# Kernel optimization log

Measured on AMD Instinct MI355X. Metric: run time of the kernel, lower is better.

The kernel has to match this reference:

```python
import jax, jax.numpy as jnp
import numpy as np

B, Q, F, D, H = 16384, 1024, 2, 5, 4  # batch, n_qubits, n_features, depth, heads


def setup_inputs() -> dict:
    key = jax.random.key(0)
    ks = iter(jax.random.split(key, 16))
    def rnd(shape, s=0.02):
        return jax.random.normal(next(ks), shape, dtype=jnp.float32) * s
    return {
        "x": jax.random.normal(next(ks), (B, F), dtype=jnp.float32),
        # amplitude_encoder: Linear(F,4Q) -> LN -> GELU -> Linear(4Q,2Q) -> LN -> Tanh -> Linear(2Q,Q)
        "amp_W1": rnd((4 * Q, F)), "amp_b1": jnp.zeros((4 * Q,), jnp.float32),
        "amp_g1": jnp.ones((4 * Q,), jnp.float32), "amp_be1": jnp.zeros((4 * Q,), jnp.float32),
        "amp_W2": rnd((2 * Q, 4 * Q)), "amp_b2": jnp.zeros((2 * Q,), jnp.float32),
        "amp_g2": jnp.ones((2 * Q,), jnp.float32), "amp_be2": jnp.zeros((2 * Q,), jnp.float32),
        "amp_W3": rnd((Q, 2 * Q)), "amp_b3": jnp.zeros((Q,), jnp.float32),
        # phase_encoder: Linear(F,2Q) -> LN -> SiLU -> Linear(2Q,Q) -> Tanh
        "ph_W1": rnd((2 * Q, F)), "ph_b1": jnp.zeros((2 * Q,), jnp.float32),
        "ph_g1": jnp.ones((2 * Q,), jnp.float32), "ph_be1": jnp.zeros((2 * Q,), jnp.float32),
        "ph_W2": rnd((Q, 2 * Q)), "ph_b2": jnp.zeros((Q,), jnp.float32),
        # rotation parameters (depth, Q, 3); only the last depth slice survives the overwrite loop
        "rot_freq": jax.random.normal(next(ks), (D, Q, 3), dtype=jnp.float32),
        "rot_phase": jax.random.normal(next(ks), (D, Q, 3), dtype=jnp.float32),
        # MultiheadAttention(Q, 4 heads)
        "attn_in_w": rnd((3 * Q, Q)), "attn_in_b": jnp.zeros((3 * Q,), jnp.float32),
        "attn_out_w": rnd((Q, Q)), "attn_out_b": jnp.zeros((Q,), jnp.float32),
    }


def _ln(x, g, b):
    m = jnp.mean(x, -1, keepdims=True)
    v = jnp.mean((x - m) ** 2, -1, keepdims=True)
    return (x - m) * jax.lax.rsqrt(v + 1e-5) * g + b


def reference(x, amp_W1, amp_b1, amp_g1, amp_be1, amp_W2, amp_b2, amp_g2, amp_be2,
              amp_W3, amp_b3, ph_W1, ph_b1, ph_g1, ph_be1, ph_W2, ph_b2,
              rot_freq, rot_phase, attn_in_w, attn_in_b, attn_out_w, attn_out_b):
    # amplitude encoder (Dropout is identity in eval mode)
    h = jax.nn.gelu(_ln(x @ amp_W1.T + amp_b1, amp_g1, amp_be1), approximate=False)
    h = jnp.tanh(_ln(h @ amp_W2.T + amp_b2, amp_g2, amp_be2))
    amp = h @ amp_W3.T + amp_b3                      # (B, Q)
    # phase encoder
    p = jax.nn.silu(_ln(x @ ph_W1.T + ph_b1, ph_g1, ph_be1))
    phase = jnp.tanh(p @ ph_W2.T + ph_b2)            # (B, Q)
    # multiscale conv branch: n_features=2 < min kernel size 3 => skipped, combined_conv = 0
    # depth loop overwrites quantum_state each iteration => only depth index D-1 matters
    rx = jnp.sin(amp * rot_freq[-1, :, 0] + rot_phase[-1, :, 0])
    ry = jnp.cos(phase * rot_freq[-1, :, 1] + rot_phase[-1, :, 1])
    rz = jnp.broadcast_to(jnp.tanh(rot_phase[-1, :, 2]), rx.shape)  # tanh(0*f + p)
    qs = (rx + ry + rz) / 3.0                        # (B, Q)
    # MultiheadAttention with seq_len == 1: softmax over a single key is exactly 1,
    # so attended output == V projection regardless of Q/K.
    qkv = qs @ attn_in_w.T + attn_in_b               # (B, 3Q)
    v = qkv[:, 2 * Q:]                               # (B, Q)
    return v @ attn_out_w.T + attn_out_b
```

## Files before the change

### kernel.cpp

```cpp
#include <hip/hip_runtime.h>

using bf16x8 = __attribute__((ext_vector_type(8))) __bf16;
using u16x8  = __attribute__((ext_vector_type(8))) unsigned short;
using f32x4  = __attribute__((ext_vector_type(4))) float;

__device__ __forceinline__ unsigned short f2bf(float f){
  unsigned int u = __float_as_uint(f);
  u += 0x7fffu + ((u >> 16) & 1u);
  return (unsigned short)(u >> 16);
}
__device__ __forceinline__ float bf2f(unsigned short h){
  return __uint_as_float(((unsigned int)h) << 16);
}

__global__ __launch_bounds__(256) void cvt_bf16(const float* __restrict__ s,
                                                unsigned short* __restrict__ d, int n){
  int i = blockIdx.x * 256 + threadIdx.x;
  if (i < n) d[i] = f2bf(s[i]);
}

__global__ __launch_bounds__(256) void front_amp_kernel(
    const float* __restrict__ x,
    const float* __restrict__ W1, const float* __restrict__ b1,
    const float* __restrict__ g1, const float* __restrict__ be1,
    unsigned short* __restrict__ h)
{
  __shared__ float red[256];
  __shared__ float red2[256];
  __shared__ float s_mean, s_inv;
  const int row = blockIdx.x;
  const int tid = threadIdx.x;
  const float x0 = x[row * 2 + 0];
  const float x1 = x[row * 2 + 1];

  const f32x4* W4 = (const f32x4*)(W1 + (size_t)tid * 32);
  float va[16];
  float sum = 0.f, sq = 0.f;
#pragma unroll
  for (int i4 = 0; i4 < 4; i4++){
    f32x4 b4 = *(const f32x4*)(b1 + tid * 16 + i4 * 4);
    f32x4 wa = W4[i4 * 2], wb = W4[i4 * 2 + 1];
    float v0 = x0 * wa[0] + x1 * wa[1] + b4[0];
    float v1 = x0 * wa[2] + x1 * wa[3] + b4[1];
    float v2 = x0 * wb[0] + x1 * wb[1] + b4[2];
    float v3 = x0 * wb[2] + x1 * wb[3] + b4[3];
    va[i4*4+0] = v0; va[i4*4+1] = v1; va[i4*4+2] = v2; va[i4*4+3] = v3;
    sum += v0 + v1 + v2 + v3;
    sq  += v0*v0 + v1*v1 + v2*v2 + v3*v3;
  }
  red[tid] = sum; red2[tid] = sq; __syncthreads();
  for (int s = 128; s > 0; s >>= 1){
    if (tid < s){ red[tid] += red[tid + s]; red2[tid] += red2[tid + s]; }
    __syncthreads();
  }
  if (tid == 0){
    float m = red[0] * (1.0f / 4096.0f);
    float v = red2[0] * (1.0f / 4096.0f) - m * m;
    s_mean = m; s_inv = rsqrtf(v + 1e-5f);
  }
  __syncthreads();
  float mean = s_mean, inv = s_inv;
#pragma unroll
  for (int i8 = 0; i8 < 2; i8++){
    f32x4 ga = *(const f32x4*)(g1  + tid * 16 + i8 * 8);
    f32x4 gb = *(const f32x4*)(g1  + tid * 16 + i8 * 8 + 4);
    f32x4 ba = *(const f32x4*)(be1 + tid * 16 + i8 * 8);
    f32x4 bb = *(const f32x4*)(be1 + tid * 16 + i8 * 8 + 4);
    u16x8 o;
#pragma unroll
    for (int k = 0; k < 8; k++){
      float gk = (k < 4) ? ga[k] : gb[k - 4];
      float bk = (k < 4) ? ba[k] : bb[k - 4];
      float y = (va[i8 * 8 + k] - mean) * inv * gk + bk;
      float ge = 0.5f * y * (1.0f + erff(y * 0.70710678118654752f));
      o[k] = f2bf(ge);
    }
    *(u16x8*)&h[(size_t)row * 4096 + tid * 16 + i8 * 8] = o;
  }
}

__global__ __launch_bounds__(256) void front_ph_kernel(
    const float* __restrict__ x,
    const float* __restrict__ W1, const float* __restrict__ b1,
    const float* __restrict__ g1, const float* __restrict__ be1,
    unsigned short* __restrict__ p)
{
  __shared__ float red[256];
  __shared__ float red2[256];
  __shared__ float s_mean, s_inv;
  const int row = blockIdx.x;
  const int tid = threadIdx.x;
  const float x0 = x[row * 2 + 0];
  const float x1 = x[row * 2 + 1];

  const f32x4* W4 = (const f32x4*)(W1 + (size_t)tid * 16);
  float vp[8];
  float sum = 0.f, sq = 0.f;
#pragma unroll
  for (int i4 = 0; i4 < 2; i4++){
    f32x4 b4 = *(const f32x4*)(b1 + tid * 8 + i4 * 4);
    f32x4 wa = W4[i4 * 2], wb = W4[i4 * 2 + 1];
    float v0 = x0 * wa[0] + x1 * wa[1] + b4[0];
    float v1 = x0 * wa[2] + x1 * wa[3] + b4[1];
    float v2 = x0 * wb[0] + x1 * wb[1] + b4[2];
    float v3 = x0 * wb[2] + x1 * wb[3] + b4[3];
    vp[i4*4+0] = v0; vp[i4*4+1] = v1; vp[i4*4+2] = v2; vp[i4*4+3] = v3;
    sum += v0 + v1 + v2 + v3;
    sq  += v0*v0 + v1*v1 + v2*v2 + v3*v3;
  }
  red[tid] = sum; red2[tid] = sq; __syncthreads();
  for (int s = 128; s > 0; s >>= 1){
    if (tid < s){ red[tid] += red[tid + s]; red2[tid] += red2[tid + s]; }
    __syncthreads();
  }
  if (tid == 0){
    float m = red[0] * (1.0f / 2048.0f);
    float v = red2[0] * (1.0f / 2048.0f) - m * m;
    s_mean = m; s_inv = rsqrtf(v + 1e-5f);
  }
  __syncthreads();
  float mean = s_mean, inv = s_inv;
  {
    f32x4 ga = *(const f32x4*)(g1  + tid * 8);
    f32x4 gb = *(const f32x4*)(g1  + tid * 8 + 4);
    f32x4 ba = *(const f32x4*)(be1 + tid * 8);
    f32x4 bb = *(const f32x4*)(be1 + tid * 8 + 4);
    u16x8 o;
#pragma unroll
    for (int k = 0; k < 8; k++){
      float gk = (k < 4) ? ga[k] : gb[k - 4];
      float bk = (k < 4) ? ba[k] : bb[k - 4];
      float y = (vp[k] - mean) * inv * gk + bk;
      float si = y / (1.0f + expf(-y));
      o[k] = f2bf(si);
    }
    *(u16x8*)&p[(size_t)row * 2048 + tid * 8] = o;
  }
}

__global__ __launch_bounds__(256) void ln_tanh_kernel(
    unsigned short* __restrict__ c, const float* __restrict__ g,
    const float* __restrict__ be)
{
  __shared__ float red[256];
  __shared__ float red2[256];
  __shared__ float s_mean, s_inv;
  const size_t base = (size_t)blockIdx.x * 2048;
  const int tid = threadIdx.x;
  u16x8 cv = *(const u16x8*)&c[base + tid * 8];
  float v[8];
  float sum = 0.f, sq = 0.f;
#pragma unroll
  for (int k = 0; k < 8; k++){
    float t = bf2f(cv[k]);
    v[k] = t; sum += t; sq += t * t;
  }
  red[tid] = sum; red2[tid] = sq; __syncthreads();
  for (int s = 128; s > 0; s >>= 1){
    if (tid < s){ red[tid] += red[tid + s]; red2[tid] += red2[tid + s]; }
    __syncthreads();
  }
  if (tid == 0){
    float m = red[0] * (1.0f / 2048.0f);
    float vv = red2[0] * (1.0f / 2048.0f) - m * m;
    s_mean = m; s_inv = rsqrtf(vv + 1e-5f);
  }
  __syncthreads();
  float mean = s_mean, inv = s_inv;
  {
    f32x4 ga = *(const f32x4*)(g  + tid * 8);
    f32x4 gb = *(const f32x4*)(g  + tid * 8 + 4);
    f32x4 ba = *(const f32x4*)(be + tid * 8);
    f32x4 bb = *(const f32x4*)(be + tid * 8 + 4);
    u16x8 o;
#pragma unroll
    for (int k = 0; k < 8; k++){
      float gk = (k < 4) ? ga[k] : gb[k - 4];
      float bk = (k < 4) ? ba[k] : bb[k - 4];
      float y = (v[k] - mean) * inv * gk + bk;
      o[k] = f2bf(tanhf(y));
    }
    *(u16x8*)&c[base + tid * 8] = o;
  }
}


#define WAITV8() asm volatile("s_waitcnt vmcnt(8)" ::: "memory")
#define WAITV4() asm volatile("s_waitcnt vmcnt(4)" ::: "memory")
#define WAITV0() asm volatile("s_waitcnt vmcnt(0)" ::: "memory")

template<int EPI>
__global__ __launch_bounds__(512, 2) void gemm_bt(
    const unsigned short* __restrict__ A, const unsigned short* __restrict__ B,
    void* __restrict__ outp, int M, int N, int K, int nT,
    const float* __restrict__ bias,
    const float* __restrict__ aux0, const float* __restrict__ aux1,
    const unsigned short* __restrict__ aux2)
{
  __shared__ __align__(16) char smem_raw[131072];
  unsigned short* S = (unsigned short*)smem_raw;

  const int tid  = threadIdx.x;
  const int wave = tid >> 6, lane = tid & 63;
  const int wm = wave >> 1, wn = wave & 1;
  const int lm = lane & 15, lq = lane >> 4;

  int lid = blockIdx.x;
  {
    const int nwg = gridDim.x;
    if ((nwg & 7) == 0) lid = (lid & 7) * (nwg >> 3) + (lid >> 3);
  }
  const int m0 = (lid / nT) * 256, n0 = (lid % nT) * 256;

  f32x4 acc[4][8];
#pragma unroll
  for (int i = 0; i < 4; i++)
#pragma unroll
    for (int j = 0; j < 8; j++) acc[i][j] = (f32x4){0.f, 0.f, 0.f, 0.f};

  const int lr = lane >> 2;
  const int lc = (((lane & 3) ^ ((lr >> 1) & 3)) << 3);
  const unsigned short* gA = A + (size_t)(m0 + wave * 32 + lr) * K + lc;
  const unsigned short* gB = B + (size_t)(n0 + wave * 32 + lr) * K + lc;
  const size_t rowK16 = (size_t)16 * K;

  auto stage = [&](int buf){
    unsigned short* lA = S + buf * 16384 + wave * 1024;
    unsigned short* lB = lA + 8192;
    __builtin_amdgcn_global_load_lds(
        (const __attribute__((address_space(1))) void*)gA,
        (__attribute__((address_space(3))) void*)lA, 16, 0, 0);
    __builtin_amdgcn_global_load_lds(
        (const __attribute__((address_space(1))) void*)(gA + rowK16),
        (__attribute__((address_space(3))) void*)(lA + 512), 16, 0, 0);
    __builtin_amdgcn_global_load_lds(
        (const __attribute__((address_space(1))) void*)gB,
        (__attribute__((address_space(3))) void*)lB, 16, 0, 0);
    __builtin_amdgcn_global_load_lds(
        (const __attribute__((address_space(1))) void*)(gB + rowK16),
        (__attribute__((address_space(3))) void*)(lB + 512), 16, 0, 0);
    gA += 32; gB += 32;
  };

  const int nTk = K >> 5;
  stage(0); stage(1); stage(2);
  for (int t = 0; t < nTk; ++t){
    if (t + 2 < nTk)      WAITV8();
    else if (t + 1 < nTk) WAITV4();
    else                  WAITV0();
    __builtin_amdgcn_s_barrier();
    if (t + 3 < nTk) stage((t + 3) & 3);

    const int buf = t & 3;
    const unsigned short* sA = S + buf * 16384;
    const unsigned short* sB = sA + 8192;
    bf16x8 af[4], bfr[4];
#pragma unroll
    for (int q = 0; q < 4; q++){
      const int r = wm * 64 + q * 16 + lm;
      af[q] = *(const bf16x8*)&sA[r * 32 + ((lq ^ ((r >> 1) & 3)) << 3)];
    }
#pragma unroll
    for (int q = 0; q < 4; q++){
      const int r = wn * 128 + q * 16 + lm;
      bfr[q] = *(const bf16x8*)&sB[r * 32 + ((lq ^ ((r >> 1) & 3)) << 3)];
    }
    __builtin_amdgcn_s_setprio(1);
#pragma unroll
    for (int i = 0; i < 4; i++)
#pragma unroll
      for (int j = 0; j < 4; j++)
        acc[i][j] = __builtin_amdgcn_mfma_f32_16x16x32_bf16(af[i], bfr[j], acc[i][j], 0, 0, 0);
    __builtin_amdgcn_s_setprio(0);
    __builtin_amdgcn_sched_barrier(0);
    __builtin_amdgcn_s_barrier();
    __builtin_amdgcn_sched_barrier(0);
#pragma unroll
    for (int q = 0; q < 4; q++){
      const int r = wn * 128 + 64 + q * 16 + lm;
      bfr[q] = *(const bf16x8*)&sB[r * 32 + ((lq ^ ((r >> 1) & 3)) << 3)];
    }
    __builtin_amdgcn_s_setprio(1);
#pragma unroll
    for (int i = 0; i < 4; i++)
#pragma unroll
      for (int j = 0; j < 4; j++)
        acc[i][j + 4] = __builtin_amdgcn_mfma_f32_16x16x32_bf16(af[i], bfr[j], acc[i][j + 4], 0, 0, 0);
    __builtin_amdgcn_s_setprio(0);
  }

  __syncthreads();
  float* ew = (float*)smem_raw + wave * 2112;

#pragma unroll
  for (int i = 0; i < 4; i++){
#pragma unroll
    for (int j = 0; j < 8; j++){
      const int col = n0 + wn * 128 + j * 16 + lm;
      float bcol = bias[col];
      float f0 = 0.f, p0 = 0.f, rzv = 0.f;
      if constexpr (EPI == 1){
        f0 = aux0[3 * col]; p0 = aux1[3 * col]; rzv = tanhf(aux1[3 * col + 2]);
      }
      if constexpr (EPI == 2){
        f0 = aux0[3 * col + 1]; p0 = aux1[3 * col + 1];
      }
#pragma unroll
      for (int r = 0; r < 4; r++){
        const float val = acc[i][j][r];
        float pre;
        if constexpr (EPI == 0 || EPI == 3)      pre = val + bcol;
        else if constexpr (EPI == 1)             pre = sinf((val + bcol) * f0 + p0) + rzv;
        else                                     pre = cosf(tanhf(val + bcol) * f0 + p0);
        ew[(lq * 4 + r) * 132 + j * 16 + lm] = pre;
      }
    }
    if constexpr (EPI != 3){
#pragma unroll
      for (int s = 0; s < 4; s++){
        const int lrow = 4 * s + lq;
        const int grow = m0 + wm * 64 + i * 16 + lrow;
        const float* src = ew + lrow * 132 + lm * 8;
        f32x4 v0 = *(const f32x4*)(src);
        f32x4 v1 = *(const f32x4*)(src + 4);
        const size_t gidx = (size_t)grow * N + n0 + wn * 128 + lm * 8;
        u16x8 o;
        if constexpr (EPI == 1){
          u16x8 ry8 = *(const u16x8*)&aux2[gidx];
#pragma unroll
          for (int t = 0; t < 4; t++){
            o[t]     = f2bf((v0[t] + bf2f(ry8[t]))     * (1.0f / 3.0f));
            o[t + 4] = f2bf((v1[t] + bf2f(ry8[t + 4])) * (1.0f / 3.0f));
          }
        } else {
#pragma unroll
          for (int t = 0; t < 4; t++){
            o[t] = f2bf(v0[t]); o[t + 4] = f2bf(v1[t]);
          }
        }
        *(u16x8*)&((unsigned short*)outp)[gidx] = o;
      }
    } else {
#pragma unroll
      for (int s = 0; s < 8; s++){
        const int lrow = 2 * s + (lane >> 5);
        const int grow = m0 + wm * 64 + i * 16 + lrow;
        const int lcol = (lane & 31) * 4;
        f32x4 v = *(const f32x4*)(ew + lrow * 132 + lcol);
        *(f32x4*)&((float*)outp)[(size_t)grow * N + n0 + wn * 128 + lcol] = v;
      }
    }
  }
}

extern "C" void kernel_launch(void* const* d_in, const int* in_sizes, int n_in,
                              void* d_out, int out_size, void* d_ws, size_t ws_size,
                              hipStream_t stream)
{
  const float* x    = (const float*)d_in[0];
  const float* aW1  = (const float*)d_in[1];
  const float* ab1  = (const float*)d_in[2];
  const float* ag1  = (const float*)d_in[3];
  const float* abe1 = (const float*)d_in[4];
  const float* aW2  = (const float*)d_in[5];
  const float* ab2  = (const float*)d_in[6];
  const float* ag2  = (const float*)d_in[7];
  const float* abe2 = (const float*)d_in[8];
  const float* aW3  = (const float*)d_in[9];
  const float* ab3  = (const float*)d_in[10];
  const float* pW1  = (const float*)d_in[11];
  const float* pb1  = (const float*)d_in[12];
  const float* pg1  = (const float*)d_in[13];
  const float* pbe1 = (const float*)d_in[14];
  const float* pW2  = (const float*)d_in[15];
  const float* pb2  = (const float*)d_in[16];
  const float* rfreq  = (const float*)d_in[17];
  const float* rphase = (const float*)d_in[18];
  const float* aiw  = (const float*)d_in[19];
  const float* aib  = (const float*)d_in[20];
  const float* aow  = (const float*)d_in[21];
  const float* aob  = (const float*)d_in[22];

  const int B = 16384, Q = 1024;

  char* ws = (char*)d_ws;
  size_t off = 0;
  auto alloc = [&](size_t bytes) -> char* {
    char* ptr = ws + off; off += (bytes + 255) & ~(size_t)255; return ptr;
  };
  unsigned short* Wb2  = (unsigned short*)alloc((size_t)2 * Q * 4 * Q * 2);
  unsigned short* Wb3  = (unsigned short*)alloc((size_t)Q * 2 * Q * 2);
  unsigned short* PWb2 = (unsigned short*)alloc((size_t)Q * 2 * Q * 2);
  unsigned short* WVb  = (unsigned short*)alloc((size_t)Q * Q * 2);
  unsigned short* WOb  = (unsigned short*)alloc((size_t)Q * Q * 2);
  unsigned short* R1   = (unsigned short*)alloc((size_t)B * 4 * Q * 2);
  unsigned short* ry   = (unsigned short*)alloc((size_t)B * Q * 2);

  unsigned short* p  = R1;
  unsigned short* h  = R1;
  unsigned short* qs = R1;
  unsigned short* v  = R1 + (size_t)B * Q;
  unsigned short* c2 = (unsigned short*)d_out;

  cvt_bf16<<<(2*Q*4*Q + 255) / 256, 256, 0, stream>>>(aW2, Wb2, 2*Q*4*Q);
  cvt_bf16<<<(Q*2*Q + 255) / 256, 256, 0, stream>>>(aW3, Wb3, Q*2*Q);
  cvt_bf16<<<(Q*2*Q + 255) / 256, 256, 0, stream>>>(pW2, PWb2, Q*2*Q);
  cvt_bf16<<<(Q*Q + 255) / 256, 256, 0, stream>>>(aiw + (size_t)2*Q*Q, WVb, Q*Q);
  cvt_bf16<<<(Q*Q + 255) / 256, 256, 0, stream>>>(aow, WOb, Q*Q);

  const float* rf4 = rfreq  + (size_t)4 * Q * 3;
  const float* rp4 = rphase + (size_t)4 * Q * 3;

  const int mT = B / 256;
  const int nT1 = 2 * Q / 256;
  const int nTq = Q / 256;

  front_ph_kernel<<<B, 256, 0, stream>>>(x, pW1, pb1, pg1, pbe1, p);
  gemm_bt<2><<<nTq * mT, 512, 0, stream>>>(p, PWb2, ry, B, Q, 2*Q, nTq,
                                           pb2, rf4, rp4, nullptr);

  front_amp_kernel<<<B, 256, 0, stream>>>(x, aW1, ab1, ag1, abe1, h);
  gemm_bt<0><<<nT1 * mT, 512, 0, stream>>>(h, Wb2, c2, B, 2*Q, 4*Q, nT1,
                                           ab2, nullptr, nullptr, nullptr);
  ln_tanh_kernel<<<B, 256, 0, stream>>>(c2, ag2, abe2);

  gemm_bt<1><<<nTq * mT, 512, 0, stream>>>(c2, Wb3, qs, B, Q, 2*Q, nTq,
                                           ab3, rf4, rp4, ry);
  gemm_bt<0><<<nTq * mT, 512, 0, stream>>>(qs, WVb, v, B, Q, Q, nTq,
                                           aib + 2*Q, nullptr, nullptr, nullptr);
  gemm_bt<3><<<nTq * mT, 512, 0, stream>>>(v, WOb, d_out, B, Q, Q, nTq,
                                           aob, nullptr, nullptr, nullptr);
}
```

Before: 924.2 us.

## Restructure GEMM main loop to prefetch B fragments one stage ahead with double registers

The K loop of the bf16 MFMA GEMM is unrolled by two and keeps two register sets of B fragments (8 each), so the next tile's B fragments are read from LDS while the current tile's 32 MFMAs issue. The previous mid-tile barrier and split B read are removed, giving one barrier per K-tile. This aims to hide LDS read latency behind MFMA work, at the cost of higher VGPR pressure under launch bounds (512,2) and an assumption that the tile count is even.

```diff
diff --git a/kernel.cpp b/kernel.cpp
--- a/kernel.cpp
+++ b/kernel.cpp
@@ -185,8 +185,8 @@
 }
 
 
+#define WAITV4() asm volatile("s_waitcnt vmcnt(4)" ::: "memory")
 #define WAITV8() asm volatile("s_waitcnt vmcnt(8)" ::: "memory")
-#define WAITV4() asm volatile("s_waitcnt vmcnt(4)" ::: "memory")
 #define WAITV0() asm volatile("s_waitcnt vmcnt(0)" ::: "memory")
 
 template<int EPI>
@@ -242,51 +242,54 @@
     gA += 32; gB += 32;
   };
 
-  const int nTk = K >> 5;
-  stage(0); stage(1); stage(2);
-  for (int t = 0; t < nTk; ++t){
-    if (t + 2 < nTk)      WAITV8();
-    else if (t + 1 < nTk) WAITV4();
-    else                  WAITV0();
-    __builtin_amdgcn_s_barrier();
-    if (t + 3 < nTk) stage((t + 3) & 3);
-
-    const int buf = t & 3;
+  auto readA = [&](int buf, bf16x8* af){
     const unsigned short* sA = S + buf * 16384;
-    const unsigned short* sB = sA + 8192;
-    bf16x8 af[4], bfr[4];
 #pragma unroll
     for (int q = 0; q < 4; q++){
       const int r = wm * 64 + q * 16 + lm;
       af[q] = *(const bf16x8*)&sA[r * 32 + ((lq ^ ((r >> 1) & 3)) << 3)];
     }
-#pragma unroll
-    for (int q = 0; q < 4; q++){
+  };
+  auto readB = [&](int buf, bf16x8* bfr){
+    const unsigned short* sB = S + buf * 16384 + 8192;
+#pragma unroll
+    for (int q = 0; q < 8; q++){
       const int r = wn * 128 + q * 16 + lm;
       bfr[q] = *(const bf16x8*)&sB[r * 32 + ((lq ^ ((r >> 1) & 3)) << 3)];
     }
+  };
+
+  auto mfmaAll = [&](const bf16x8* af, const bf16x8* bfr){
     __builtin_amdgcn_s_setprio(1);
 #pragma unroll
     for (int i = 0; i < 4; i++)
 #pragma unroll
-      for (int j = 0; j < 4; j++)
+      for (int j = 0; j < 8; j++)
         acc[i][j] = __builtin_amdgcn_mfma_f32_16x16x32_bf16(af[i], bfr[j], acc[i][j], 0, 0, 0);
     __builtin_amdgcn_s_setprio(0);
-    __builtin_amdgcn_sched_barrier(0);
+  };
+
+  const int nTk = K >> 5;
+  bf16x8 af[4], bfA[8], bfB[8];
+  stage(0); stage(1); stage(2);
+  WAITV8();
+  __builtin_amdgcn_s_barrier();
+  readB(0, bfA);
+  for (int t = 0; t < nTk; t += 2){
+    if (t + 2 < nTk) WAITV4(); else WAITV0();
     __builtin_amdgcn_s_barrier();
-    __builtin_amdgcn_sched_barrier(0);
-#pragma unroll
-    for (int q = 0; q < 4; q++){
-      const int r = wn * 128 + 64 + q * 16 + lm;
-      bfr[q] = *(const bf16x8*)&sB[r * 32 + ((lq ^ ((r >> 1) & 3)) << 3)];
-    }
-    __builtin_amdgcn_s_setprio(1);
-#pragma unroll
-    for (int i = 0; i < 4; i++)
-#pragma unroll
-      for (int j = 0; j < 4; j++)
-        acc[i][j + 4] = __builtin_amdgcn_mfma_f32_16x16x32_bf16(af[i], bfr[j], acc[i][j + 4], 0, 0, 0);
-    __builtin_amdgcn_s_setprio(0);
+    if (t + 3 < nTk) stage((t + 3) & 3);
+    readB((t + 1) & 3, bfB);
+    readA(t & 3, af);
+    mfmaAll(af, bfA);
+    if (t + 2 < nTk){
+      if (t + 3 < nTk) WAITV4(); else WAITV0();
+    }
+    __builtin_amdgcn_s_barrier();
+    if (t + 4 < nTk) stage((t + 4) & 3);
+    if (t + 2 < nTk) readB((t + 2) & 3, bfA);
+    readA((t + 1) & 3, af);
+    mfmaAll(af, bfB);
   }
 
   __syncthreads();
```

New measurement: 907.3 us. No clear change (-1.8%).
